# Kernel optimization log

Measured on AMD Instinct MI355X. Metric: run time of the kernel, lower is better.

## Reference

```python
import jax, jax.numpy as jnp
import numpy as np

NUM_BOXES = 512
NUM_COORDS = 200000
C = 128
MAX_SELECTED = 262144  # static pad size for the ragged output
P_INSIDE = 0.002       # expected ~204.8k selected rows < MAX_SELECTED


def setup_inputs() -> dict:
    key = jax.random.key(0)
    k1, k2, k3 = jax.random.split(key, 3)
    coords = jax.random.randint(k1, (NUM_COORDS, 4), 0, 256, dtype=jnp.int32)
    features = jax.random.normal(k2, (NUM_COORDS, C), dtype=jnp.float32)
    is_inside = jax.random.uniform(k3, (NUM_BOXES, NUM_COORDS)) < P_INSIDE
    return {"coords": coords, "features": features, "is_inside": is_inside,
            "max_selected": MAX_SELECTED}


def reference(coords, features, is_inside, max_selected):
    # Faithful to select_coords/select_features, but WITHOUT materializing the
    # dense (num_boxes, num_coords, C) expand: compute flat nonzero indices of
    # the mask directly and gather once. Output is padded to a static size
    # (padded rows zeroed) since jax requires static shapes.
    num_boxes, num_coords = is_inside.shape
    total = num_boxes * num_coords
    flat_idx = jnp.nonzero(is_inside.ravel(), size=max_selected, fill_value=total)[0]
    valid = flat_idx < total                      # [K] pad mask
    safe = jnp.where(valid, flat_idx, 0)
    box_idx = (safe // num_coords).astype(jnp.int32)   # [K]
    coord_idx = safe % num_coords                       # [K]
    # select_features: features[None].expand(...)[is_inside]
    selected_features = jnp.where(valid[:, None], features[coord_idx], 0.0)  # [K, C]
    # select_coords: cat(coords[:, :-1] gathered, box index)
    sel_xyz = coords[coord_idx, :-1]                    # [K, 3]
    ext_coords = jnp.concatenate([sel_xyz, box_idx[:, None]], axis=-1)  # [K, 4]
    extended_coordinates = jnp.where(valid[:, None], ext_coords, 0)
    return extended_coordinates, selected_features
```

## Files before the change

kernel.cpp:

```cpp
#include <hip/hip_runtime.h>


#define BS  256
#define WPB 1024
#define DETB 32

__device__ __forceinline__ unsigned nzmask4(unsigned v){
  unsigned t = (v | ((v & 0x7f7f7f7fu) + 0x7f7f7f7fu)) & 0x80808080u;
  return ((t >> 7) & 1u) | ((t >> 14) & 2u) | ((t >> 21) & 4u) | ((t >> 28) & 8u);
}
__device__ __forceinline__ unsigned nzmask16(uint4 x){
  return nzmask4(x.x) | (nzmask4(x.y) << 4) | (nzmask4(x.z) << 8) | (nzmask4(x.w) << 12);
}

__global__ void detect_mode(const uchar4* p, int nvec, int* flags){
  int found = 0;
  for (int i = blockIdx.x*blockDim.x + threadIdx.x; i < nvec;
       i += gridDim.x*blockDim.x){
    uchar4 v = p[i];
    if (v.y) found = 1;
  }
  __shared__ int sh;
  if (threadIdx.x == 0) sh = 0;
  __syncthreads();
  if (found) atomicOr(&sh, 1);
  __syncthreads();
  if (threadIdx.x == 0) flags[blockIdx.x] = sh;
}

__global__ void pack_count(const void* data, const int* flags,
                           long long totalElems, int wordsTotal,
                           unsigned* maskOut, int* counts){
  __shared__ int modeSh;
  if (threadIdx.x == 0){
    int f = 0;
    for (int i = 0; i < DETB; ++i) f |= flags[i];
    modeSh = f;
  }
  __syncthreads();
  const bool byteMode = (modeSh != 0);
  const int tid = threadIdx.x;
  int cnt = 0;
  const int wBase = blockIdx.x * WPB;
  if (byteMode){
    const uint4* d = (const uint4*)data;
    const unsigned char* p8 = (const unsigned char*)data;
    for (int i = tid; i < WPB; i += BS){
      const int w = wBase + i;
      if (w >= wordsTotal) break;
      const long long e0 = (long long)w << 5;
      unsigned m;
      if (e0 + 31 < totalElems){
        uint4 a = d[2*w], b = d[2*w+1];
        m = nzmask16(a) | (nzmask16(b) << 16);
      } else {
        m = 0;
        for (int b = 0; b < 32 && e0 + b < totalElems; ++b)
          if (p8[e0 + b]) m |= (1u << b);
      }
      maskOut[w] = m;
      cnt += __popc(m);
    }
  } else {
    const uint4* d = (const uint4*)data;
    const unsigned* p32 = (const unsigned*)data;
    for (int i = tid; i < WPB; i += BS){
      const int w = wBase + i;
      if (w >= wordsTotal) break;
      const long long e0 = (long long)w << 5;
      unsigned m = 0;
      if (e0 + 31 < totalElems){
        #pragma unroll
        for (int k = 0; k < 8; ++k){
          uint4 x = d[8*(long long)w + k];
          m |= ((unsigned)(x.x!=0) << (4*k)) | ((unsigned)(x.y!=0) << (4*k+1)) |
               ((unsigned)(x.z!=0) << (4*k+2)) | ((unsigned)(x.w!=0) << (4*k+3));
        }
      } else {
        for (int b = 0; b < 32 && e0 + b < totalElems; ++b)
          if (p32[e0 + b]) m |= (1u << b);
      }
      maskOut[w] = m;
      cnt += __popc(m);
    }
  }
  const int lane = tid & 63, wid = tid >> 6;
  for (int off = 32; off > 0; off >>= 1) cnt += __shfl_down(cnt, off, 64);
  __shared__ int wsum[BS/64];
  if (lane == 0) wsum[wid] = cnt;
  __syncthreads();
  if (tid == 0){
    int s = 0;
    for (int w = 0; w < BS/64; ++w) s += wsum[w];
    counts[blockIdx.x] = s;
  }
}

__global__ void scan_kernel(const int* counts, int* offsets, int* totalOut, int nb){
  const int tid = threadIdx.x;
  const int per = (nb + BS - 1)/BS;
  const int base = tid*per;
  int vals[16];
  int sum = 0;
  for (int k = 0; k < per; ++k){
    int idx = base + k;
    int c = (idx < nb) ? counts[idx] : 0;
    vals[k] = sum; sum += c;
  }
  int incl = sum;
  const int lane = tid & 63, wid = tid >> 6;
  for (int off = 1; off < 64; off <<= 1){
    int t = __shfl_up(incl, off, 64);
    if (lane >= off) incl += t;
  }
  __shared__ int wsum[BS/64];
  if (lane == 63) wsum[wid] = incl;
  __syncthreads();
  int wbase = 0;
  for (int w = 0; w < wid; ++w) wbase += wsum[w];
  const int excl = wbase + incl - sum;
  for (int k = 0; k < per; ++k){
    int idx = base + k;
    if (idx < nb) offsets[idx] = excl + vals[k];
  }
  if (tid == BS-1){
    int t = 0;
    for (int w = 0; w < BS/64; ++w) t += wsum[w];
    *totalOut = t;
  }
}

__global__ void emit_kernel(const unsigned* mask, const int* offsets,
                            int wordsTotal, int max_sel, int* outIdx){
  const int tid = threadIdx.x;
  const int lane = tid & 63, wid = tid >> 6;
  const int wBase = blockIdx.x * WPB;
  int running = offsets[blockIdx.x];
  __shared__ int wsum[BS/64];
  const int iters = WPB / BS;
  for (int it = 0; it < iters; ++it){
    const int w = wBase + it*BS + tid;
    unsigned m = (w < wordsTotal) ? mask[w] : 0u;
    const int cnt = __popc(m);
    int incl = cnt;
    for (int off = 1; off < 64; off <<= 1){
      int t = __shfl_up(incl, off, 64);
      if (lane >= off) incl += t;
    }
    if (lane == 63) wsum[wid] = incl;
    __syncthreads();
    int wbase = 0;
    for (int ww = 0; ww < wid; ++ww) wbase += wsum[ww];
    int iterTotal = 0;
    for (int ww = 0; ww < BS/64; ++ww) iterTotal += wsum[ww];
    int pos = running + wbase + incl - cnt;
    if (m){
      const long long e0 = (long long)w << 5;
      unsigned mm = m;
      while (mm){
        const int b = __ffs(mm) - 1;
        mm &= mm - 1;
        if (pos < max_sel) outIdx[pos] = (int)(e0 + b);
        ++pos;
      }
    }
    running += iterTotal;
    __syncthreads();
  }
}

__global__ void gather_kernel(const int* selIdx, const int* totalPtr,
                              const int4* coords, const float4* feat,
                              int num_coords, int c4, int max_sel,
                              float4* outExt, float4* outFeat){
  const int lane    = threadIdx.x & 31;
  const int g0      = (blockIdx.x*blockDim.x + threadIdx.x) >> 5;
  const int gstride = (gridDim.x*blockDim.x) >> 5;
  int total = *totalPtr;
  if (total > max_sel) total = max_sel;
  const float4 z = make_float4(0.f, 0.f, 0.f, 0.f);
  for (int r = g0; r < max_sel; r += gstride){
    float4* dst = outFeat + (long long)r*c4;
    if (r < total){
      const int flat = selIdx[r];
      const unsigned box = (unsigned)flat / (unsigned)num_coords;
      const int ci = flat - (int)box*num_coords;
      const float4* src = feat + (long long)ci*c4;
      for (int c = lane; c < c4; c += 32) dst[c] = src[c];
      if (lane == 0){
        int4 cc = coords[ci];
        outExt[r] = make_float4((float)cc.x, (float)cc.y, (float)cc.z, (float)box);
      }
    } else {
      for (int c = lane; c < c4; c += 32) dst[c] = z;
      if (lane == 0) outExt[r] = z;
    }
  }
}

extern "C" void kernel_launch(void* const* d_in, const int* in_sizes, int n_in,
                              void* d_out, int out_size, void* d_ws, size_t ws_size,
                              hipStream_t stream){
  const int*   coords   = (const int*)d_in[0];
  const float* features = (const float*)d_in[1];
  const void*  inside   = d_in[2];

  const int num_coords = in_sizes[0] / 4;
  const int C          = in_sizes[1] / num_coords;
  const int c4         = C / 4;
  const long long totalElems = (long long)in_sizes[2];
  const int max_sel    = out_size / (4 + C);

  const int wordsTotal = (int)((totalElems + 31) / 32);
  const int NBP        = (wordsTotal + WPB - 1) / WPB;

  int* ws      = (int*)d_ws;
  int* flags   = ws;
  int* total   = ws + DETB;
  int* counts  = ws + DETB + 1;
  int* offsets = counts + NBP;
  int* selIdx  = offsets + NBP;
  unsigned* maskBuf = (unsigned*)(selIdx + max_sel);

  hipLaunchKernelGGL(detect_mode, dim3(DETB), dim3(BS), 0, stream,
                     (const uchar4*)inside, 65536 , flags);
  hipLaunchKernelGGL(pack_count, dim3(NBP), dim3(BS), 0, stream,
                     inside, flags, totalElems, wordsTotal, maskBuf, counts);
  hipLaunchKernelGGL(scan_kernel, dim3(1), dim3(BS), 0, stream,
                     counts, offsets, total, NBP);
  hipLaunchKernelGGL(emit_kernel, dim3(NBP), dim3(BS), 0, stream,
                     maskBuf, offsets, wordsTotal, max_sel, selIdx);
  hipLaunchKernelGGL(gather_kernel, dim3(2048), dim3(BS), 0, stream,
                     selIdx, total, (const int4*)coords, (const float4*)features,
                     num_coords, c4, max_sel,
                     (float4*)d_out,
                     (float4*)((float*)d_out + (long long)max_sel*4));
}
```

Before: 667.2 us.

## Fuse mask pack, scan and emit into single-pass decoupled-lookback compaction

```diff
diff --git a/kernel.cpp b/kernel.cpp
--- a/kernel.cpp
+++ b/kernel.cpp
@@ -1,151 +1,121 @@
 #include <hip/hip_runtime.h>
 
 
-#define BS  256
-#define WPB 1024
-#define DETB 32
-
-__device__ __forceinline__ unsigned nzmask4(unsigned v){
-  unsigned t = (v | ((v & 0x7f7f7f7fu) + 0x7f7f7f7fu)) & 0x80808080u;
-  return ((t >> 7) & 1u) | ((t >> 14) & 2u) | ((t >> 21) & 4u) | ((t >> 28) & 8u);
-}
-__device__ __forceinline__ unsigned nzmask16(uint4 x){
-  return nzmask4(x.x) | (nzmask4(x.y) << 4) | (nzmask4(x.z) << 8) | (nzmask4(x.w) << 12);
-}
-
-__global__ void detect_mode(const uchar4* p, int nvec, int* flags){
-  int found = 0;
-  for (int i = blockIdx.x*blockDim.x + threadIdx.x; i < nvec;
-       i += gridDim.x*blockDim.x){
-    uchar4 v = p[i];
-    if (v.y) found = 1;
-  }
-  __shared__ int sh;
-  if (threadIdx.x == 0) sh = 0;
+#define BS   256
+#define WPT  8
+#define WPB  (BS*WPT)
+#define FLAG_AGG (1ull<<62)
+#define FLAG_PRE (2ull<<62)
+
+__global__ void __launch_bounds__(BS) compact_lookback(
+    const uint4* __restrict__ d, long long totalElems, int wordsTotal,
+    int numTiles, int max_sel,
+    unsigned long long* __restrict__ state,
+    int* __restrict__ ticketPtr,
+    int* __restrict__ selIdx, int* __restrict__ totalOut)
+{
+  __shared__ int sh_ticket;
+  __shared__ int sh_excl;
+  __shared__ int wsum[BS/64];
+  const int tid  = threadIdx.x;
+  const int lane = tid & 63;
+  const int wid  = tid >> 6;
+
+  if (tid == 0) sh_ticket = atomicAdd(ticketPtr, 1);
   __syncthreads();
-  if (found) atomicOr(&sh, 1);
-  __syncthreads();
-  if (threadIdx.x == 0) flags[blockIdx.x] = sh;
-}
-
-__global__ void pack_count(const void* data, const int* flags,
-                           long long totalElems, int wordsTotal,
-                           unsigned* maskOut, int* counts){
-  __shared__ int modeSh;
-  if (threadIdx.x == 0){
-    int f = 0;
-    for (int i = 0; i < DETB; ++i) f |= flags[i];
-    modeSh = f;
-  }
-  __syncthreads();
-  const bool byteMode = (modeSh != 0);
-  const int tid = threadIdx.x;
+  const int t     = sh_ticket;
+  const int wBase = t * WPB;
+
+  unsigned m[WPT];
   int cnt = 0;
-  const int wBase = blockIdx.x * WPB;
-  if (byteMode){
-    const uint4* d = (const uint4*)data;
-    const unsigned char* p8 = (const unsigned char*)data;
-    for (int i = tid; i < WPB; i += BS){
-      const int w = wBase + i;
-      if (w >= wordsTotal) break;
+  #pragma unroll
+  for (int k = 0; k < WPT; ++k){
+    const int w = wBase + k*BS + tid;
+    unsigned mm = 0;
+    if (w < wordsTotal){
       const long long e0 = (long long)w << 5;
-      unsigned m;
       if (e0 + 31 < totalElems){
-        uint4 a = d[2*w], b = d[2*w+1];
-        m = nzmask16(a) | (nzmask16(b) << 16);
-      } else {
-        m = 0;
-        for (int b = 0; b < 32 && e0 + b < totalElems; ++b)
-          if (p8[e0 + b]) m |= (1u << b);
-      }
-      maskOut[w] = m;
-      cnt += __popc(m);
-    }
-  } else {
-    const uint4* d = (const uint4*)data;
-    const unsigned* p32 = (const unsigned*)data;
-    for (int i = tid; i < WPB; i += BS){
-      const int w = wBase + i;
-      if (w >= wordsTotal) break;
-      const long long e0 = (long long)w << 5;
-      unsigned m = 0;
-      if (e0 + 31 < totalElems){
+        const uint4* base = d + 8*(long long)w;
         #pragma unroll
-        for (int k = 0; k < 8; ++k){
-          uint4 x = d[8*(long long)w + k];
-          m |= ((unsigned)(x.x!=0) << (4*k)) | ((unsigned)(x.y!=0) << (4*k+1)) |
-               ((unsigned)(x.z!=0) << (4*k+2)) | ((unsigned)(x.w!=0) << (4*k+3));
+        for (int q = 0; q < 8; ++q){
+          uint4 x = base[q];
+          mm |= ((unsigned)(x.x!=0) << (4*q))   | ((unsigned)(x.y!=0) << (4*q+1)) |
+                ((unsigned)(x.z!=0) << (4*q+2)) | ((unsigned)(x.w!=0) << (4*q+3));
         }
       } else {
-        for (int b = 0; b < 32 && e0 + b < totalElems; ++b)
-          if (p32[e0 + b]) m |= (1u << b);
-      }
-      maskOut[w] = m;
-      cnt += __popc(m);
-    }
-  }
-  const int lane = tid & 63, wid = tid >> 6;
-  for (int off = 32; off > 0; off >>= 1) cnt += __shfl_down(cnt, off, 64);
-  __shared__ int wsum[BS/64];
-  if (lane == 0) wsum[wid] = cnt;
+        const unsigned* p32 = (const unsigned*)d;
+        for (int b2 = 0; b2 < 32 && e0 + b2 < totalElems; ++b2)
+          if (p32[e0 + b2]) mm |= (1u << b2);
+      }
+    }
+    m[k] = mm;
+    cnt += __popc(mm);
+  }
+
+  int red = cnt;
+  for (int off = 32; off > 0; off >>= 1) red += __shfl_down(red, off, 64);
+  if (lane == 0) wsum[wid] = red;
   __syncthreads();
+  const int agg = wsum[0] + wsum[1] + wsum[2] + wsum[3];
+
   if (tid == 0){
-    int s = 0;
-    for (int w = 0; w < BS/64; ++w) s += wsum[w];
-    counts[blockIdx.x] = s;
-  }
-}
-
-__global__ void scan_kernel(const int* counts, int* offsets, int* totalOut, int nb){
-  const int tid = threadIdx.x;
-  const int per = (nb + BS - 1)/BS;
-  const int base = tid*per;
-  int vals[16];
-  int sum = 0;
-  for (int k = 0; k < per; ++k){
-    int idx = base + k;
-    int c = (idx < nb) ? counts[idx] : 0;
-    vals[k] = sum; sum += c;
-  }
-  int incl = sum;
-  const int lane = tid & 63, wid = tid >> 6;
-  for (int off = 1; off < 64; off <<= 1){
-    int t = __shfl_up(incl, off, 64);
-    if (lane >= off) incl += t;
-  }
-  __shared__ int wsum[BS/64];
-  if (lane == 63) wsum[wid] = incl;
+    unsigned long long p = (t == 0 ? FLAG_PRE : FLAG_AGG) | (unsigned long long)(unsigned)agg;
+    __hip_atomic_store(&state[t], p, __ATOMIC_RELEASE, __HIP_MEMORY_SCOPE_AGENT);
+    if (t == 0){
+      sh_excl = 0;
+      if (numTiles == 1) *totalOut = agg;
+    }
+  }
+  if (t > 0 && wid == 0){
+    int run = 0;
+    int j = t - 1;
+    while (true){
+      const int idx = j - lane;
+      unsigned long long s;
+      if (idx >= 0){
+        s = __hip_atomic_load(&state[idx], __ATOMIC_ACQUIRE, __HIP_MEMORY_SCOPE_AGENT);
+        while (s == 0ull){
+          __builtin_amdgcn_s_sleep(2);
+          s = __hip_atomic_load(&state[idx], __ATOMIC_ACQUIRE, __HIP_MEMORY_SCOPE_AGENT);
+        }
+      } else {
+        s = FLAG_PRE;
+      }
+      const unsigned long long ball = __ballot((s >> 62) == 2ull);
+      const int val = (int)(s & 0xFFFFFFFFull);
+      int contrib;
+      int stop = 0;
+      if (ball){
+        const int firstPre = __ffsll((long long)ball) - 1;
+        contrib = (lane <= firstPre) ? val : 0;
+        stop = 1;
+      } else {
+        contrib = val;
+      }
+      for (int off = 32; off > 0; off >>= 1) contrib += __shfl_down(contrib, off, 64);
+      if (lane == 0) run += contrib;
+      if (stop) break;
+      j -= 64;
+    }
+    if (lane == 0){
+      sh_excl = run;
+      __hip_atomic_store(&state[t],
+                         FLAG_PRE | (unsigned long long)(unsigned)(run + agg),
+                         __ATOMIC_RELEASE, __HIP_MEMORY_SCOPE_AGENT);
+      if (t == numTiles - 1) *totalOut = run + agg;
+    }
+  }
   __syncthreads();
-  int wbase = 0;
-  for (int w = 0; w < wid; ++w) wbase += wsum[w];
-  const int excl = wbase + incl - sum;
-  for (int k = 0; k < per; ++k){
-    int idx = base + k;
-    if (idx < nb) offsets[idx] = excl + vals[k];
-  }
-  if (tid == BS-1){
-    int t = 0;
-    for (int w = 0; w < BS/64; ++w) t += wsum[w];
-    *totalOut = t;
-  }
-}
-
-__global__ void emit_kernel(const unsigned* mask, const int* offsets,
-                            int wordsTotal, int max_sel, int* outIdx){
-  const int tid = threadIdx.x;
-  const int lane = tid & 63, wid = tid >> 6;
-  const int wBase = blockIdx.x * WPB;
-  int running = offsets[blockIdx.x];
-  __shared__ int wsum[BS/64];
-  const int iters = WPB / BS;
-  for (int it = 0; it < iters; ++it){
-    const int w = wBase + it*BS + tid;
-    unsigned m = (w < wordsTotal) ? mask[w] : 0u;
-    const int cnt = __popc(m);
-    int incl = cnt;
+
+  int running = sh_excl;
+  #pragma unroll
+  for (int k = 0; k < WPT; ++k){
+    unsigned mm = m[k];
+    const int c = __popc(mm);
+    int incl = c;
     for (int off = 1; off < 64; off <<= 1){
-      int t = __shfl_up(incl, off, 64);
-      if (lane >= off) incl += t;
+      int tv = __shfl_up(incl, off, 64);
+      if (lane >= off) incl += tv;
     }
     if (lane == 63) wsum[wid] = incl;
     __syncthreads();
@@ -153,14 +123,14 @@
     for (int ww = 0; ww < wid; ++ww) wbase += wsum[ww];
     int iterTotal = 0;
     for (int ww = 0; ww < BS/64; ++ww) iterTotal += wsum[ww];
-    int pos = running + wbase + incl - cnt;
-    if (m){
+    int pos = running + wbase + incl - c;
+    if (mm){
+      const int w = wBase + k*BS + tid;
       const long long e0 = (long long)w << 5;
-      unsigned mm = m;
       while (mm){
         const int b = __ffs(mm) - 1;
         mm &= mm - 1;
-        if (pos < max_sel) outIdx[pos] = (int)(e0 + b);
+        if (pos < max_sel) selIdx[pos] = (int)(e0 + b);
         ++pos;
       }
     }
@@ -169,10 +139,12 @@
   }
 }
 
-__global__ void gather_kernel(const int* selIdx, const int* totalPtr,
-                              const int4* coords, const float4* feat,
-                              int num_coords, int c4, int max_sel,
-                              float4* outExt, float4* outFeat){
+__global__ void __launch_bounds__(BS) gather_kernel(
+    const int* __restrict__ selIdx, const int* __restrict__ totalPtr,
+    const int4* __restrict__ coords, const float4* __restrict__ feat,
+    int num_coords, int c4, int max_sel,
+    float4* __restrict__ outExt, float4* __restrict__ outFeat)
+{
   const int lane    = threadIdx.x & 31;
   const int g0      = (blockIdx.x*blockDim.x + threadIdx.x) >> 5;
   const int gstride = (gridDim.x*blockDim.x) >> 5;
@@ -212,24 +184,19 @@
   const int max_sel    = out_size / (4 + C);
 
   const int wordsTotal = (int)((totalElems + 31) / 32);
-  const int NBP        = (wordsTotal + WPB - 1) / WPB;
-
-  int* ws      = (int*)d_ws;
-  int* flags   = ws;
-  int* total   = ws + DETB;
-  int* counts  = ws + DETB + 1;
-  int* offsets = counts + NBP;
-  int* selIdx  = offsets + NBP;
-  unsigned* maskBuf = (unsigned*)(selIdx + max_sel);
-
-  hipLaunchKernelGGL(detect_mode, dim3(DETB), dim3(BS), 0, stream,
-                     (const uchar4*)inside, 65536 , flags);
-  hipLaunchKernelGGL(pack_count, dim3(NBP), dim3(BS), 0, stream,
-                     inside, flags, totalElems, wordsTotal, maskBuf, counts);
-  hipLaunchKernelGGL(scan_kernel, dim3(1), dim3(BS), 0, stream,
-                     counts, offsets, total, NBP);
-  hipLaunchKernelGGL(emit_kernel, dim3(NBP), dim3(BS), 0, stream,
-                     maskBuf, offsets, wordsTotal, max_sel, selIdx);
+  const int numTiles   = (wordsTotal + WPB - 1) / WPB;
+
+  unsigned long long* state = (unsigned long long*)d_ws;
+  int* ticket = (int*)(state + numTiles);
+  int* total  = ticket + 1;
+  int* selIdx = ticket + 2;
+
+  hipMemsetAsync(state, 0, (size_t)numTiles*8 + 8, stream);
+
+  hipLaunchKernelGGL(compact_lookback, dim3(numTiles), dim3(BS), 0, stream,
+                     (const uint4*)inside, totalElems, wordsTotal, numTiles, max_sel,
+                     state, ticket, selIdx, total);
+
   hipLaunchKernelGGL(gather_kernel, dim3(2048), dim3(BS), 0, stream,
                      selIdx, total, (const int4*)coords, (const float4*)features,
                      num_coords, c4, max_sel,
```

After: 888.7 us. 33.2% more time.
